# Performance work log

Hardware: AMD Instinct MI355X
Metric: run time of the kernel (lower is better)

The kernel has to match this reference:

```python
import jax, jax.numpy as jnp
import numpy as np

N_NODES = 100000
N_EDGES = 1600000
IN_DIM = 128
HID = 128
NUM_LAYERS = 3


def _sage_conv(h, src, dst, Wl, Wr, b, n_nodes):
    # PyG SAGEConv (aggr='mean'): out = lin_l(mean_j x_j) + lin_r(x_i)
    agg = jax.ops.segment_sum(h[src], dst, num_segments=n_nodes)
    cnt = jax.ops.segment_sum(jnp.ones((src.shape[0],), dtype=h.dtype), dst,
                              num_segments=n_nodes)
    mean = agg / jnp.maximum(cnt, 1.0)[:, None]
    return mean @ Wl + h @ Wr + b


def setup_inputs() -> dict:
    key = jax.random.key(0)
    ks = jax.random.split(key, 16)
    x = jax.random.normal(ks[0], (N_NODES, IN_DIM), dtype=jnp.float32)
    edge_index = jax.random.randint(ks[1], (2, N_EDGES), 0, N_NODES, dtype=jnp.int32)
    reranker_scores = jax.random.normal(ks[2], (N_NODES,), dtype=jnp.float32)
    inp = {"x": x, "edge_index": edge_index, "reranker_scores": reranker_scores}
    dims = [IN_DIM, HID, HID]
    for i in range(NUM_LAYERS):
        d_in = dims[i]
        s = 1.0 / np.sqrt(d_in)
        inp[f"Wl{i}"] = jax.random.uniform(ks[3 + 3 * i], (d_in, HID), jnp.float32, -s, s)
        inp[f"Wr{i}"] = jax.random.uniform(ks[4 + 3 * i], (d_in, HID), jnp.float32, -s, s)
        inp[f"b{i}"] = jax.random.uniform(ks[5 + 3 * i], (HID,), jnp.float32, -s, s)
    sh = 1.0 / np.sqrt(HID * NUM_LAYERS)
    inp["Ws"] = jax.random.uniform(ks[12], (HID * NUM_LAYERS, 1), jnp.float32, -sh, sh)
    inp["bs"] = jax.random.uniform(ks[13], (1,), jnp.float32, -sh, sh)
    inp["alpha"] = jnp.asarray(0.65, dtype=jnp.float32)
    return inp


def reference(x, edge_index, reranker_scores,
              Wl0, Wr0, b0, Wl1, Wr1, b1, Wl2, Wr2, b2,
              Ws, bs, alpha):
    src, dst = edge_index[0], edge_index[1]
    n = x.shape[0]
    params = [(Wl0, Wr0, b0), (Wl1, Wr1, b1), (Wl2, Wr2, b2)]
    xs = []
    h = x
    for (Wl, Wr, b) in params:
        h = jax.nn.relu(_sage_conv(h, src, dst, Wl, Wr, b, n))
        # dropout: eval-mode identity
        xs.append(h)
    hj = jnp.concatenate(xs, axis=-1)                 # [N, HID*NUM_LAYERS]
    gnn_scores = (hj @ Ws + bs)[:, 0]                 # [N]
    a = jax.nn.sigmoid(alpha)
    return a * reranker_scores + (1.0 - a) * gnn_scores
```

## Files before the change

kernel.cpp:

```cpp
#include <hip/hip_runtime.h>
#include <hip/hip_bf16.h>
#include <cstdint>

#define N_NODES 100000
#define HID 128
#define NBINS 391
#define CHUNK 4096

typedef __attribute__((ext_vector_type(8))) short short8v;
typedef __attribute__((ext_vector_type(4))) float floatx4;

__device__ __forceinline__ float bflo(unsigned v) { return __uint_as_float(v << 16); }
__device__ __forceinline__ float bfhi(unsigned v) { return __uint_as_float(v & 0xffff0000u); }
__device__ __forceinline__ unsigned short f2bf(float f) {
    unsigned u = __float_as_uint(f);
    unsigned r = (u + 0x7fffu + ((u >> 16) & 1u)) >> 16;
    return (unsigned short)r;
}

__global__ __launch_bounds__(256) void prep_kernel(const float* __restrict__ x,
                                                   unsigned short* __restrict__ xb,
                                                   const float* __restrict__ Wl0, const float* __restrict__ Wr0,
                                                   const float* __restrict__ Wl1, const float* __restrict__ Wr1,
                                                   const float* __restrict__ Wl2, const float* __restrict__ Wr2,
                                                   unsigned short* __restrict__ Bp,
                                                   const int* __restrict__ dst,
                                                   int* __restrict__ cntMat, int E) {
    __shared__ int lcnt[512];
    const int bid = blockIdx.x;
    const int tid = threadIdx.x;
    if (bid < 6250) {
        int i = bid * 256 + tid;
        const float4* p = (const float4*)x + (size_t)i * 2;
        float4 a = p[0], b = p[1];
        uint4 o;
        o.x = f2bf(a.x) | ((unsigned)f2bf(a.y) << 16);
        o.y = f2bf(a.z) | ((unsigned)f2bf(a.w) << 16);
        o.z = f2bf(b.x) | ((unsigned)f2bf(b.y) << 16);
        o.w = f2bf(b.z) | ((unsigned)f2bf(b.w) << 16);
        *(uint4*)(xb + (size_t)i * 8) = o;
    } else if (bid < 6298) {
        int idx = (bid - 6250) * 256 + tid;
        if (idx >= 12288) return;
        int g = idx & 3, c = (idx >> 2) & 127, s = (idx >> 9) & 3, t = (idx >> 11) & 1, L = idx >> 12;
        const float* W = (t == 0) ? (L == 0 ? Wl0 : (L == 1 ? Wl1 : Wl2))
                                  : (L == 0 ? Wr0 : (L == 1 ? Wr1 : Wr2));
        int k0 = s * 32 + g * 8;
        uint4 o;
        o.x = f2bf(W[(k0 + 0) * 128 + c]) | ((unsigned)f2bf(W[(k0 + 1) * 128 + c]) << 16);
        o.y = f2bf(W[(k0 + 2) * 128 + c]) | ((unsigned)f2bf(W[(k0 + 3) * 128 + c]) << 16);
        o.z = f2bf(W[(k0 + 4) * 128 + c]) | ((unsigned)f2bf(W[(k0 + 5) * 128 + c]) << 16);
        o.w = f2bf(W[(k0 + 6) * 128 + c]) | ((unsigned)f2bf(W[(k0 + 7) * 128 + c]) << 16);
        size_t chunk = (((size_t)(L * 2 + t) * 4 + s) * 128 + c) * 4 + g;
        *(uint4*)(Bp + chunk * 8) = o;
    } else {
        const int row = bid - 6298;
        lcnt[tid] = 0; lcnt[tid + 256] = 0;
        __syncthreads();
        int base = row * CHUNK;
        int end = base + CHUNK; if (end > E) end = E;
        for (int i = base + tid; i < end; i += 256) atomicAdd(&lcnt[dst[i] >> 8], 1);
        __syncthreads();
        for (int j = tid; j < NBINS; j += 256) cntMat[(size_t)row * NBINS + j] = lcnt[j];
    }
}


__global__ __launch_bounds__(512) void colscan_kernel(int* __restrict__ cntMat,
                                                      int* __restrict__ binCnt, int nch) {
    __shared__ int wsum[8];
    const int j = blockIdx.x;
    const int tid = threadIdx.x;
    const int lane = tid & 63, w = tid >> 6;
    int v = (tid < nch) ? cntMat[(size_t)tid * NBINS + j] : 0;
    int s = v;
    #pragma unroll
    for (int o = 1; o < 64; o <<= 1) {
        int t = __shfl_up(s, o, 64);
        if (lane >= o) s += t;
    }
    if (lane == 63) wsum[w] = s;
    __syncthreads();
    if (w == 0 && lane < 8) {
        int t = wsum[lane];
        int ss = t;
        #pragma unroll
        for (int o = 1; o < 8; o <<= 1) {
            int u = __shfl_up(ss, o, 64);
            if (lane >= o) ss += u;
        }
        wsum[lane] = ss - t;
    }
    __syncthreads();
    int excl = (s - v) + wsum[w];
    if (tid < nch) cntMat[(size_t)tid * NBINS + j] = excl;
    if (tid == 511) binCnt[j] = excl + v;
}

__global__ __launch_bounds__(512) void binbase_kernel(const int* __restrict__ binCnt,
                                                      int* __restrict__ binBase,
                                                      int* __restrict__ offs, int E) {
    __shared__ int wsum[8];
    const int tid = threadIdx.x;
    const int lane = tid & 63, w = tid >> 6;
    int v = (tid < NBINS) ? binCnt[tid] : 0;
    int s = v;
    #pragma unroll
    for (int o = 1; o < 64; o <<= 1) {
        int t = __shfl_up(s, o, 64);
        if (lane >= o) s += t;
    }
    if (lane == 63) wsum[w] = s;
    __syncthreads();
    if (w == 0 && lane < 8) {
        int t = wsum[lane];
        int ss = t;
        #pragma unroll
        for (int o = 1; o < 8; o <<= 1) {
            int u = __shfl_up(ss, o, 64);
            if (lane >= o) ss += u;
        }
        wsum[lane] = ss - t;
    }
    __syncthreads();
    if (tid < NBINS) binBase[tid] = (s - v) + wsum[w];
    if (tid == 0) offs[N_NODES] = E;
}

__global__ __launch_bounds__(256) void binscat_kernel(const int* __restrict__ src, const int* __restrict__ dst,
                                                      const int* __restrict__ cntMat,
                                                      const int* __restrict__ binBase,
                                                      unsigned* __restrict__ binned, int E) {
    __shared__ int cur[512];
    const int tid = threadIdx.x;
    const int row = blockIdx.x;
    for (int j = tid; j < NBINS; j += 256) cur[j] = cntMat[(size_t)row * NBINS + j] + binBase[j];
    __syncthreads();
    int base = row * CHUNK;
    int end = base + CHUNK; if (end > E) end = E;
    for (int i = base + tid; i < end; i += 256) {
        int d = dst[i];
        int s = src[i];
        int bin = d >> 8;
        int pos = atomicAdd(&cur[bin], 1);
        binned[pos] = (unsigned)s | ((unsigned)(d & 255) << 20);
    }
}

__global__ __launch_bounds__(256) void bincsr_kernel(const unsigned* __restrict__ binned,
                                                     const int* __restrict__ binBase, const int* __restrict__ binCnt,
                                                     int* __restrict__ esrc, int* __restrict__ offs) {
    __shared__ int h[256];
    __shared__ int cur[256];
    __shared__ int ssrc[8192];
    const int tid = threadIdx.x;
    const int bin = blockIdx.x;
    const int base = binBase[bin];
    const int cnt = binCnt[bin];
    h[tid] = 0;
    __syncthreads();
    for (int i = tid; i < cnt; i += 256) atomicAdd(&h[binned[base + i] >> 20], 1);
    __syncthreads();
    int v = h[tid];
    for (int o = 1; o < 256; o <<= 1) {
        int t = (tid >= o) ? h[tid - o] : 0;
        __syncthreads();
        h[tid] += t;
        __syncthreads();
    }
    int excl = h[tid] - v;
    cur[tid] = excl;
    int node = (bin << 8) + tid;
    if (node < N_NODES) offs[node] = base + excl;
    __syncthreads();
    for (int i = tid; i < cnt; i += 256) {
        unsigned p = binned[base + i];
        int pos = atomicAdd(&cur[p >> 20], 1);
        int s = (int)(p & 0xFFFFFu);
        if (pos < 8192) ssrc[pos] = s;
        else esrc[base + pos] = s;
    }
    __syncthreads();
    int lim = cnt < 8192 ? cnt : 8192;
    for (int i = tid; i < lim; i += 256) esrc[base + i] = ssrc[i];
}

__global__ __launch_bounds__(256) void agg_kernel(const unsigned short* __restrict__ h,
                                                  const int* __restrict__ offs,
                                                  const int* __restrict__ esrc,
                                                  unsigned short* __restrict__ mean) {
    const int lane = threadIdx.x & 63;
    const int node = blockIdx.x * 4 + (threadIdx.x >> 6);
    const int half = lane >> 5;
    const int fl = lane & 31;
    const int beg = offs[node], end = offs[node + 1];
    const int nb = end - beg;
    float a0 = 0.f, a1 = 0.f, a2 = 0.f, a3 = 0.f;
    for (int base = 0; base < nb; base += 64) {
        int m = nb - base; if (m > 64) m = 64;
        int sv = (lane < m) ? esrc[beg + base + lane] : 0;
        int j = 0;
        for (; j + 16 <= m; j += 16) {
            uint2 v[8];
            #pragma unroll
            for (int p = 0; p < 8; ++p) {
                int s = __shfl(sv, j + 2 * p + half, 64);
                v[p] = *(const uint2*)(h + (size_t)s * HID + fl * 4);
            }
            #pragma unroll
            for (int p = 0; p < 8; ++p) {
                a0 += bflo(v[p].x); a1 += bfhi(v[p].x);
                a2 += bflo(v[p].y); a3 += bfhi(v[p].y);
            }
        }
        for (; j + 2 <= m; j += 2) {
            int s = __shfl(sv, j + half, 64);
            uint2 vv = *(const uint2*)(h + (size_t)s * HID + fl * 4);
            a0 += bflo(vv.x); a1 += bfhi(vv.x);
            a2 += bflo(vv.y); a3 += bfhi(vv.y);
        }
        if (j < m) {
            int s = __shfl(sv, j, 64);
            if (half == 0) {
                uint2 vv = *(const uint2*)(h + (size_t)s * HID + fl * 4);
                a0 += bflo(vv.x); a1 += bfhi(vv.x);
                a2 += bflo(vv.y); a3 += bfhi(vv.y);
            }
        }
    }
    a0 += __shfl_xor(a0, 32, 64);
    a1 += __shfl_xor(a1, 32, 64);
    a2 += __shfl_xor(a2, 32, 64);
    a3 += __shfl_xor(a3, 32, 64);
    if (half == 0) {
        float inv = 1.f / (float)(nb > 0 ? nb : 1);
        uint2 o;
        o.x = (unsigned)f2bf(a0 * inv) | ((unsigned)f2bf(a1 * inv) << 16);
        o.y = (unsigned)f2bf(a2 * inv) | ((unsigned)f2bf(a3 * inv) << 16);
        *(uint2*)(mean + (size_t)node * HID + fl * 4) = o;
    }
}

__global__ __launch_bounds__(256) void gemm_kernel(const unsigned short* __restrict__ Am,
                                                   const unsigned short* __restrict__ Ah,
                                                   const unsigned short* __restrict__ Bp,
                                                   const float* __restrict__ bias,
                                                   const float* __restrict__ Wsl,
                                                   unsigned short* __restrict__ hout,
                                                   float* __restrict__ score,
                                                   const float* __restrict__ rrs,
                                                   const float* __restrict__ bsp,
                                                   const float* __restrict__ alphap,
                                                   float* __restrict__ outF,
                                                   const int accum, const int writeH, const int doFinal) {
    __shared__ unsigned short At[2 * 64 * 128];
    __shared__ float sred[2][64];
    const int tid = threadIdx.x;
    const int lane = tid & 63;
    const int w = tid >> 6;
    const int wm = w & 1, wn = w >> 1;
    const int rowBase = blockIdx.x * 64;
    const int halfRow = lane & 15;
    const int g = lane >> 4;

    {
        const unsigned short* srcs[2] = { Am, Ah };
        #pragma unroll
        for (int r = 0; r < 8; ++r) {
            int c = r * 256 + tid;
            int sIdx = c >> 10;
            int rem = c & 1023;
            int row = rem >> 4, slot = rem & 15;
            int gslot = slot ^ (row & 15);
            int grow = rowBase + row; if (grow >= N_NODES) grow = N_NODES - 1;
            const unsigned short* gp = srcs[sIdx] + (size_t)grow * HID + gslot * 8;
            unsigned ldsOff = (unsigned)(r * 4096 + w * 1024);
            __builtin_amdgcn_global_load_lds((const __attribute__((address_space(1))) void*)gp,
                                             (__attribute__((address_space(3))) void*)((char*)At + ldsOff),
                                             16, 0, 0);
        }
    }
    __syncthreads();

    floatx4 acc[2][4];
    #pragma unroll
    for (int m = 0; m < 2; m++)
        #pragma unroll
        for (int n = 0; n < 4; n++) acc[m][n] = (floatx4){0.f, 0.f, 0.f, 0.f};

    #pragma unroll
    for (int t = 0; t < 2; t++) {
        #pragma unroll
        for (int s = 0; s < 4; s++) {
            int slot = (s * 4 + g) ^ halfRow;
            int row0 = wm * 32 + halfRow;
            short8v a0 = *(const short8v*)&At[t * 8192 + row0 * 128 + slot * 8];
            short8v a1 = *(const short8v*)&At[t * 8192 + (row0 + 16) * 128 + slot * 8];
            #pragma unroll
            for (int n = 0; n < 4; n++) {
                int col = wn * 64 + n * 16 + halfRow;
                short8v b = *(const short8v*)&Bp[((((size_t)(t * 4 + s)) * 128 + col) * 4 + g) * 8];
                acc[0][n] = __builtin_amdgcn_mfma_f32_16x16x32_bf16(a0, b, acc[0][n], 0, 0, 0);
                acc[1][n] = __builtin_amdgcn_mfma_f32_16x16x32_bf16(a1, b, acc[1][n], 0, 0, 0);
            }
        }
    }

    __syncthreads();

    #pragma unroll
    for (int m = 0; m < 2; m++) {
        #pragma unroll
        for (int i = 0; i < 4; i++) {
            int rloc = wm * 32 + m * 16 + g * 4 + i;
            float ps = 0.f;
            #pragma unroll
            for (int n = 0; n < 4; n++) {
                int col = wn * 64 + n * 16 + halfRow;
                float v = acc[m][n][i] + bias[col];
                v = fmaxf(v, 0.f);
                if (writeH) At[rloc * 136 + col] = f2bf(v);
                ps += v * Wsl[col];
            }
            ps += __shfl_xor(ps, 1, 64);
            ps += __shfl_xor(ps, 2, 64);
            ps += __shfl_xor(ps, 4, 64);
            ps += __shfl_xor(ps, 8, 64);
            if (halfRow == 0) sred[wn][rloc] = ps;
        }
    }
    __syncthreads();

    if (writeH) {
        #pragma unroll
        for (int p2 = 0; p2 < 4; ++p2) {
            int lin = p2 * 256 + tid;
            int row = lin >> 4, q = lin & 15;
            int grow = rowBase + row;
            if (grow < N_NODES)
                *(uint4*)(hout + (size_t)grow * HID + q * 8) = *(const uint4*)&At[row * 136 + q * 8];
        }
    }

    if (w == 0) {
        int grow = rowBase + lane;
        if (grow < N_NODES) {
            float tot = sred[0][lane] + sred[1][lane];
            if (doFinal) {
                float sc = score[grow] + tot;
                float a = 1.f / (1.f + __expf(-alphap[0]));
                outF[grow] = a * rrs[grow] + (1.f - a) * (sc + bsp[0]);
            } else {
                score[grow] = accum ? (score[grow] + tot) : tot;
            }
        }
    }
}

extern "C" void kernel_launch(void* const* d_in, const int* in_sizes, int n_in,
                              void* d_out, int out_size, void* d_ws, size_t ws_size,
                              hipStream_t stream) {
    const float* x     = (const float*)d_in[0];
    const int*   eidx  = (const int*)d_in[1];
    const float* rrs   = (const float*)d_in[2];
    const float* Wl0   = (const float*)d_in[3];
    const float* Wr0   = (const float*)d_in[4];
    const float* b0    = (const float*)d_in[5];
    const float* Wl1   = (const float*)d_in[6];
    const float* Wr1   = (const float*)d_in[7];
    const float* b1    = (const float*)d_in[8];
    const float* Wl2   = (const float*)d_in[9];
    const float* Wr2   = (const float*)d_in[10];
    const float* b2    = (const float*)d_in[11];
    const float* Ws    = (const float*)d_in[12];
    const float* bs    = (const float*)d_in[13];
    const float* alpha = (const float*)d_in[14];

    const int N = N_NODES;
    const int E = in_sizes[1] / 2;
    const int* src = eidx;
    const int* dst = eidx + E;

    uintptr_t p = (uintptr_t)d_ws;
    auto alloc = [&](size_t bytes) -> void* {
        p = (p + 255) & ~(uintptr_t)255;
        void* r = (void*)p;
        p += bytes;
        return r;
    };
    int*            offs    = (int*)alloc((size_t)(N + 1) * 4);
    int*            esrc    = (int*)alloc((size_t)E * 4);
    float*          score   = (float*)alloc((size_t)N * 4);
    int*            binBase = (int*)alloc(512 * 4);
    int*            binCnt  = (int*)alloc(512 * 4);
    unsigned short* xb      = (unsigned short*)alloc((size_t)N * HID * 2);
    unsigned short* bufA    = (unsigned short*)alloc((size_t)N * HID * 2);
    unsigned short* bufB    = (unsigned short*)alloc((size_t)N * HID * 2);
    unsigned short* Bp      = (unsigned short*)alloc((size_t)3 * 32768 * 2);

    int*      cntMat = (int*)bufA;
    unsigned* binned = (unsigned*)bufB;

    const int nch = (E + CHUNK - 1) / CHUNK;

    prep_kernel<<<6250 + 48 + nch, 256, 0, stream>>>(x, xb, Wl0, Wr0, Wl1, Wr1, Wl2, Wr2, Bp,
                                                     dst, cntMat, E);

    colscan_kernel<<<NBINS, 512, 0, stream>>>(cntMat, binCnt, nch);
    binbase_kernel<<<1, 512, 0, stream>>>(binCnt, binBase, offs, E);
    binscat_kernel<<<nch, 256, 0, stream>>>(src, dst, cntMat, binBase, binned, E);
    bincsr_kernel<<<NBINS, 256, 0, stream>>>(binned, binBase, binCnt, esrc, offs);

    const int aggGrid  = N / 4;
    const int gemmGrid = (N + 63) / 64;
    float* outF = (float*)d_out;

    agg_kernel<<<aggGrid, 256, 0, stream>>>(xb, offs, esrc, bufA);
    gemm_kernel<<<gemmGrid, 256, 0, stream>>>(bufA, xb, Bp + 0 * 32768, b0, Ws + 0 * HID, bufA, score,
                                              rrs, bs, alpha, outF, 0, 1, 0);
    agg_kernel<<<aggGrid, 256, 0, stream>>>(bufA, offs, esrc, bufB);
    gemm_kernel<<<gemmGrid, 256, 0, stream>>>(bufB, bufA, Bp + 1 * 32768, b1, Ws + 1 * HID, bufB, score,
                                              rrs, bs, alpha, outF, 1, 1, 0);
    agg_kernel<<<aggGrid, 256, 0, stream>>>(bufB, offs, esrc, bufA);
    gemm_kernel<<<gemmGrid, 256, 0, stream>>>(bufA, bufB, Bp + 2 * 32768, b2, Ws + 2 * HID, bufA, score,
                                              rrs, bs, alpha, outF, 1, 0, 1);
}
```

Measured before the change: 319.7 us.

## Store node features in feature-blocked layout for cache-friendly aggregation

Node features are stored as 8 feature blocks of 16 bf16 values, each block holding all nodes contiguously. Aggregation blocks now cover one feature block for 16 nodes, with 16 edges gathered in parallel per wavefront, so each pass touches a smaller 3.2MB slice that is more likely to stay in cache. The prep and GEMM load/store paths are rewritten to match the new layout. Each gather is now only 32 bytes per row, and every edge index is reloaded 8 times, once per feature block.

```diff
diff --git a/kernel.cpp b/kernel.cpp
--- a/kernel.cpp
+++ b/kernel.cpp
@@ -19,7 +19,7 @@
 }
 
 __global__ __launch_bounds__(256) void prep_kernel(const float* __restrict__ x,
-                                                   unsigned short* __restrict__ xb,
+                                                   unsigned short* __restrict__ xbT,
                                                    const float* __restrict__ Wl0, const float* __restrict__ Wr0,
                                                    const float* __restrict__ Wl1, const float* __restrict__ Wr1,
                                                    const float* __restrict__ Wl2, const float* __restrict__ Wr2,
@@ -30,15 +30,17 @@
     const int bid = blockIdx.x;
     const int tid = threadIdx.x;
     if (bid < 6250) {
-        int i = bid * 256 + tid;
-        const float4* p = (const float4*)x + (size_t)i * 2;
+        int idx = bid * 256 + tid;
+        int n = idx >> 4, c = idx & 15;
+        const float4* p = (const float4*)(x + (size_t)n * HID + c * 8);
         float4 a = p[0], b = p[1];
         uint4 o;
         o.x = f2bf(a.x) | ((unsigned)f2bf(a.y) << 16);
         o.y = f2bf(a.z) | ((unsigned)f2bf(a.w) << 16);
         o.z = f2bf(b.x) | ((unsigned)f2bf(b.y) << 16);
         o.w = f2bf(b.z) | ((unsigned)f2bf(b.w) << 16);
-        *(uint4*)(xb + (size_t)i * 8) = o;
+        int f = c >> 1, half = c & 1;
+        *(uint4*)(xbT + ((size_t)f * N_NODES + n) * 16 + half * 8) = o;
     } else if (bid < 6298) {
         int idx = (bid - 6250) * 256 + tid;
         if (idx >= 12288) return;
@@ -185,59 +187,49 @@
     for (int i = tid; i < lim; i += 256) esrc[base + i] = ssrc[i];
 }
 
-__global__ __launch_bounds__(256) void agg_kernel(const unsigned short* __restrict__ h,
+__global__ __launch_bounds__(256) void agg_kernel(const unsigned short* __restrict__ hT,
                                                   const int* __restrict__ offs,
                                                   const int* __restrict__ esrc,
-                                                  unsigned short* __restrict__ mean) {
+                                                  unsigned short* __restrict__ meanT) {
+    const int bid = blockIdx.x;
+    const int f = bid & 7;
+    const int nodeBase = (bid >> 3) * 16;
     const int lane = threadIdx.x & 63;
-    const int node = blockIdx.x * 4 + (threadIdx.x >> 6);
-    const int half = lane >> 5;
-    const int fl = lane & 31;
-    const int beg = offs[node], end = offs[node + 1];
-    const int nb = end - beg;
-    float a0 = 0.f, a1 = 0.f, a2 = 0.f, a3 = 0.f;
-    for (int base = 0; base < nb; base += 64) {
-        int m = nb - base; if (m > 64) m = 64;
-        int sv = (lane < m) ? esrc[beg + base + lane] : 0;
-        int j = 0;
-        for (; j + 16 <= m; j += 16) {
-            uint2 v[8];
-            #pragma unroll
-            for (int p = 0; p < 8; ++p) {
-                int s = __shfl(sv, j + 2 * p + half, 64);
-                v[p] = *(const uint2*)(h + (size_t)s * HID + fl * 4);
+    const int w = threadIdx.x >> 6;
+    const int e = lane >> 2;
+    const int q = lane & 3;
+    const unsigned short* hfb = hT + (size_t)f * N_NODES * 16;
+    unsigned short* mfb = meanT + (size_t)f * N_NODES * 16;
+
+    #pragma unroll
+    for (int k = 0; k < 4; ++k) {
+        const int node = nodeBase + w * 4 + k;
+        const int beg = offs[node], end = offs[node + 1];
+        const int nb = end - beg;
+        float a0 = 0.f, a1 = 0.f, a2 = 0.f, a3 = 0.f;
+        for (int b = 0; b < nb; b += 16) {
+            int ei = b + e;
+            if (ei < nb) {
+                int si = __builtin_nontemporal_load(esrc + beg + ei);
+                uint2 v = *(const uint2*)(hfb + (size_t)si * 16 + q * 4);
+                a0 += bflo(v.x); a1 += bfhi(v.x);
+                a2 += bflo(v.y); a3 += bfhi(v.y);
             }
-            #pragma unroll
-            for (int p = 0; p < 8; ++p) {
-                a0 += bflo(v[p].x); a1 += bfhi(v[p].x);
-                a2 += bflo(v[p].y); a3 += bfhi(v[p].y);
-            }
-        }
-        for (; j + 2 <= m; j += 2) {
-            int s = __shfl(sv, j + half, 64);
-            uint2 vv = *(const uint2*)(h + (size_t)s * HID + fl * 4);
-            a0 += bflo(vv.x); a1 += bfhi(vv.x);
-            a2 += bflo(vv.y); a3 += bfhi(vv.y);
-        }
-        if (j < m) {
-            int s = __shfl(sv, j, 64);
-            if (half == 0) {
-                uint2 vv = *(const uint2*)(h + (size_t)s * HID + fl * 4);
-                a0 += bflo(vv.x); a1 += bfhi(vv.x);
-                a2 += bflo(vv.y); a3 += bfhi(vv.y);
-            }
-        }
-    }
-    a0 += __shfl_xor(a0, 32, 64);
-    a1 += __shfl_xor(a1, 32, 64);
-    a2 += __shfl_xor(a2, 32, 64);
-    a3 += __shfl_xor(a3, 32, 64);
-    if (half == 0) {
-        float inv = 1.f / (float)(nb > 0 ? nb : 1);
-        uint2 o;
-        o.x = (unsigned)f2bf(a0 * inv) | ((unsigned)f2bf(a1 * inv) << 16);
-        o.y = (unsigned)f2bf(a2 * inv) | ((unsigned)f2bf(a3 * inv) << 16);
-        *(uint2*)(mean + (size_t)node * HID + fl * 4) = o;
+        }
+        #pragma unroll
+        for (int o = 4; o < 64; o <<= 1) {
+            a0 += __shfl_xor(a0, o, 64);
+            a1 += __shfl_xor(a1, o, 64);
+            a2 += __shfl_xor(a2, o, 64);
+            a3 += __shfl_xor(a3, o, 64);
+        }
+        if (e == 0) {
+            float inv = 1.f / (float)(nb > 0 ? nb : 1);
+            uint2 o2;
+            o2.x = (unsigned)f2bf(a0 * inv) | ((unsigned)f2bf(a1 * inv) << 16);
+            o2.y = (unsigned)f2bf(a2 * inv) | ((unsigned)f2bf(a3 * inv) << 16);
+            *(uint2*)(mfb + (size_t)node * 16 + q * 4) = o2;
+        }
     }
 }
 
@@ -273,7 +265,7 @@
             int row = rem >> 4, slot = rem & 15;
             int gslot = slot ^ (row & 15);
             int grow = rowBase + row; if (grow >= N_NODES) grow = N_NODES - 1;
-            const unsigned short* gp = srcs[sIdx] + (size_t)grow * HID + gslot * 8;
+            const unsigned short* gp = srcs[sIdx] + ((size_t)(gslot >> 1) * N_NODES + grow) * 16 + (gslot & 1) * 8;
             unsigned ldsOff = (unsigned)(r * 4096 + w * 1024);
             __builtin_amdgcn_global_load_lds((const __attribute__((address_space(1))) void*)gp,
                                              (__attribute__((address_space(3))) void*)((char*)At + ldsOff),
@@ -334,11 +326,14 @@
     if (writeH) {
         #pragma unroll
         for (int p2 = 0; p2 < 4; ++p2) {
-            int lin = p2 * 256 + tid;
-            int row = lin >> 4, q = lin & 15;
+            int idx = p2 * 256 + tid;
+            int f = idx >> 7;
+            int rem = idx & 127;
+            int row = rem >> 1, half = rem & 1;
             int grow = rowBase + row;
             if (grow < N_NODES)
-                *(uint4*)(hout + (size_t)grow * HID + q * 8) = *(const uint4*)&At[row * 136 + q * 8];
+                *(uint4*)(hout + ((size_t)f * N_NODES + grow) * 16 + half * 8) =
+                    *(const uint4*)&At[row * 136 + f * 16 + half * 8];
         }
     }
 
@@ -411,7 +406,7 @@
     binscat_kernel<<<nch, 256, 0, stream>>>(src, dst, cntMat, binBase, binned, E);
     bincsr_kernel<<<NBINS, 256, 0, stream>>>(binned, binBase, binCnt, esrc, offs);
 
-    const int aggGrid  = N / 4;
+    const int aggGrid  = 8 * (N / 16);
     const int gemmGrid = (N + 63) / 64;
     float* outF = (float*)d_out;
 
```

New measurement: 784.0 us. 145% more time.

## Process two 64-row tiles per GEMM block with staged LDS prefetch

Applied to the files above, without the earlier changes.

Each GEMM block now handles 128 rows as two 64-row groups. Both groups' A tiles are issued to LDS up front, and the first group computes after a partial vmcnt wait, so the second group's loads overlap the first group's MFMA and epilogue work. The grid is halved to match. The cost is double the LDS per block, which may lower occupancy, and a reliance on hand-written vmcnt counts that also have to account for the compiler's own global loads.

```diff
diff --git a/kernel.cpp b/kernel.cpp
--- a/kernel.cpp
+++ b/kernel.cpp
@@ -253,105 +253,118 @@
                                                    const float* __restrict__ alphap,
                                                    float* __restrict__ outF,
                                                    const int accum, const int writeH, const int doFinal) {
-    __shared__ unsigned short At[2 * 64 * 128];
+    __shared__ unsigned short At[2][2 * 64 * 128];
     __shared__ float sred[2][64];
     const int tid = threadIdx.x;
     const int lane = tid & 63;
     const int w = tid >> 6;
     const int wm = w & 1, wn = w >> 1;
-    const int rowBase = blockIdx.x * 64;
+    const int rowBase0 = blockIdx.x * 128;
     const int halfRow = lane & 15;
     const int g = lane >> 4;
 
     {
         const unsigned short* srcs[2] = { Am, Ah };
         #pragma unroll
-        for (int r = 0; r < 8; ++r) {
-            int c = r * 256 + tid;
-            int sIdx = c >> 10;
-            int rem = c & 1023;
-            int row = rem >> 4, slot = rem & 15;
-            int gslot = slot ^ (row & 15);
-            int grow = rowBase + row; if (grow >= N_NODES) grow = N_NODES - 1;
-            const unsigned short* gp = srcs[sIdx] + (size_t)grow * HID + gslot * 8;
-            unsigned ldsOff = (unsigned)(r * 4096 + w * 1024);
-            __builtin_amdgcn_global_load_lds((const __attribute__((address_space(1))) void*)gp,
-                                             (__attribute__((address_space(3))) void*)((char*)At + ldsOff),
-                                             16, 0, 0);
-        }
-    }
-    __syncthreads();
-
-    floatx4 acc[2][4];
+        for (int grp = 0; grp < 2; ++grp) {
+            #pragma unroll
+            for (int r = 0; r < 8; ++r) {
+                int c = r * 256 + tid;
+                int sIdx = c >> 10;
+                int rem = c & 1023;
+                int row = rem >> 4, slot = rem & 15;
+                int gslot = slot ^ (row & 15);
+                int grow = rowBase0 + grp * 64 + row; if (grow >= N_NODES) grow = N_NODES - 1;
+                const unsigned short* gp = srcs[sIdx] + (size_t)grow * HID + gslot * 8;
+                unsigned ldsOff = (unsigned)(grp * 32768 + r * 4096 + w * 1024);
+                __builtin_amdgcn_global_load_lds((const __attribute__((address_space(1))) void*)gp,
+                                                 (__attribute__((address_space(3))) void*)((char*)&At[0][0] + ldsOff),
+                                                 16, 0, 0);
+            }
+        }
+    }
+
     #pragma unroll
-    for (int m = 0; m < 2; m++)
-        #pragma unroll
-        for (int n = 0; n < 4; n++) acc[m][n] = (floatx4){0.f, 0.f, 0.f, 0.f};
-
-    #pragma unroll
-    for (int t = 0; t < 2; t++) {
-        #pragma unroll
-        for (int s = 0; s < 4; s++) {
-            int slot = (s * 4 + g) ^ halfRow;
-            int row0 = wm * 32 + halfRow;
-            short8v a0 = *(const short8v*)&At[t * 8192 + row0 * 128 + slot * 8];
-            short8v a1 = *(const short8v*)&At[t * 8192 + (row0 + 16) * 128 + slot * 8];
-            #pragma unroll
-            for (int n = 0; n < 4; n++) {
-                int col = wn * 64 + n * 16 + halfRow;
-                short8v b = *(const short8v*)&Bp[((((size_t)(t * 4 + s)) * 128 + col) * 4 + g) * 8];
-                acc[0][n] = __builtin_amdgcn_mfma_f32_16x16x32_bf16(a0, b, acc[0][n], 0, 0, 0);
-                acc[1][n] = __builtin_amdgcn_mfma_f32_16x16x32_bf16(a1, b, acc[1][n], 0, 0, 0);
-            }
-        }
-    }
-
-    __syncthreads();
-
-    #pragma unroll
-    for (int m = 0; m < 2; m++) {
-        #pragma unroll
-        for (int i = 0; i < 4; i++) {
-            int rloc = wm * 32 + m * 16 + g * 4 + i;
-            float ps = 0.f;
-            #pragma unroll
-            for (int n = 0; n < 4; n++) {
-                int col = wn * 64 + n * 16 + halfRow;
-                float v = acc[m][n][i] + bias[col];
-                v = fmaxf(v, 0.f);
-                if (writeH) At[rloc * 136 + col] = f2bf(v);
-                ps += v * Wsl[col];
-            }
-            ps += __shfl_xor(ps, 1, 64);
-            ps += __shfl_xor(ps, 2, 64);
-            ps += __shfl_xor(ps, 4, 64);
-            ps += __shfl_xor(ps, 8, 64);
-            if (halfRow == 0) sred[wn][rloc] = ps;
-        }
-    }
-    __syncthreads();
-
-    if (writeH) {
-        #pragma unroll
-        for (int p2 = 0; p2 < 4; ++p2) {
-            int lin = p2 * 256 + tid;
-            int row = lin >> 4, q = lin & 15;
-            int grow = rowBase + row;
-            if (grow < N_NODES)
-                *(uint4*)(hout + (size_t)grow * HID + q * 8) = *(const uint4*)&At[row * 136 + q * 8];
-        }
-    }
-
-    if (w == 0) {
-        int grow = rowBase + lane;
-        if (grow < N_NODES) {
-            float tot = sred[0][lane] + sred[1][lane];
-            if (doFinal) {
-                float sc = score[grow] + tot;
-                float a = 1.f / (1.f + __expf(-alphap[0]));
-                outF[grow] = a * rrs[grow] + (1.f - a) * (sc + bsp[0]);
-            } else {
-                score[grow] = accum ? (score[grow] + tot) : tot;
+    for (int grp = 0; grp < 2; ++grp) {
+        if (grp == 0) { asm volatile("s_waitcnt vmcnt(8)" ::: "memory"); }
+        else         { asm volatile("s_waitcnt vmcnt(0)" ::: "memory"); }
+        __builtin_amdgcn_s_barrier();
+        __builtin_amdgcn_sched_barrier(0);
+
+        const int rowBase = rowBase0 + grp * 64;
+        unsigned short* Atg = &At[grp][0];
+
+        floatx4 acc[2][4];
+        #pragma unroll
+        for (int m = 0; m < 2; m++)
+            #pragma unroll
+            for (int n = 0; n < 4; n++) acc[m][n] = (floatx4){0.f, 0.f, 0.f, 0.f};
+
+        #pragma unroll
+        for (int t = 0; t < 2; t++) {
+            #pragma unroll
+            for (int s = 0; s < 4; s++) {
+                int slot = (s * 4 + g) ^ halfRow;
+                int row0 = wm * 32 + halfRow;
+                short8v a0 = *(const short8v*)&Atg[t * 8192 + row0 * 128 + slot * 8];
+                short8v a1 = *(const short8v*)&Atg[t * 8192 + (row0 + 16) * 128 + slot * 8];
+                #pragma unroll
+                for (int n = 0; n < 4; n++) {
+                    int col = wn * 64 + n * 16 + halfRow;
+                    short8v b = *(const short8v*)&Bp[((((size_t)(t * 4 + s)) * 128 + col) * 4 + g) * 8];
+                    acc[0][n] = __builtin_amdgcn_mfma_f32_16x16x32_bf16(a0, b, acc[0][n], 0, 0, 0);
+                    acc[1][n] = __builtin_amdgcn_mfma_f32_16x16x32_bf16(a1, b, acc[1][n], 0, 0, 0);
+                }
+            }
+        }
+
+        __syncthreads();
+
+        #pragma unroll
+        for (int m = 0; m < 2; m++) {
+            #pragma unroll
+            for (int i = 0; i < 4; i++) {
+                int rloc = wm * 32 + m * 16 + g * 4 + i;
+                float ps = 0.f;
+                #pragma unroll
+                for (int n = 0; n < 4; n++) {
+                    int col = wn * 64 + n * 16 + halfRow;
+                    float v = acc[m][n][i] + bias[col];
+                    v = fmaxf(v, 0.f);
+                    if (writeH) Atg[rloc * 136 + col] = f2bf(v);
+                    ps += v * Wsl[col];
+                }
+                ps += __shfl_xor(ps, 1, 64);
+                ps += __shfl_xor(ps, 2, 64);
+                ps += __shfl_xor(ps, 4, 64);
+                ps += __shfl_xor(ps, 8, 64);
+                if (halfRow == 0) sred[wn][rloc] = ps;
+            }
+        }
+        __syncthreads();
+
+        if (writeH) {
+            #pragma unroll
+            for (int p2 = 0; p2 < 4; ++p2) {
+                int lin = p2 * 256 + tid;
+                int row = lin >> 4, q = lin & 15;
+                int grow = rowBase + row;
+                if (grow < N_NODES)
+                    *(uint4*)(hout + (size_t)grow * HID + q * 8) = *(const uint4*)&Atg[row * 136 + q * 8];
+            }
+        }
+
+        if (w == 0) {
+            int grow = rowBase + lane;
+            if (grow < N_NODES) {
+                float tot = sred[0][lane] + sred[1][lane];
+                if (doFinal) {
+                    float sc = score[grow] + tot;
+                    float a = 1.f / (1.f + __expf(-alphap[0]));
+                    outF[grow] = a * rrs[grow] + (1.f - a) * (sc + bsp[0]);
+                } else {
+                    score[grow] = accum ? (score[grow] + tot) : tot;
+                }
             }
         }
     }
@@ -412,7 +425,7 @@
     bincsr_kernel<<<NBINS, 256, 0, stream>>>(binned, binBase, binCnt, esrc, offs);
 
     const int aggGrid  = N / 4;
-    const int gemmGrid = (N + 63) / 64;
+    const int gemmGrid = (N + 127) / 128;
     float* outF = (float*)d_out;
 
     agg_kernel<<<aggGrid, 256, 0, stream>>>(xb, offs, esrc, bufA);
```

Measured after the change: 336.0 us. +5.1%, slower.
